# Performance work log

Measured on AMD Instinct MI355X. Metric: run time of the kernel, lower is better.

Reference implementation:

```python
import jax, jax.numpy as jnp
import numpy as np


def hadamard_transform(x):
    """Normalized fast Walsh-Hadamard transform along the last axis.

    Equivalent to x @ H_n / sqrt(n) with H_n the Sylvester Hadamard matrix.
    Last dim must be a power of two. Computed in fp32 (rotate_fp32=True).
    """
    orig_dtype = x.dtype
    x = x.astype(jnp.float32)
    n = x.shape[-1]
    lead = x.shape[:-1]
    x = x.reshape(-1, n)  # (B, n)
    h = 1
    while h < n:
        # butterfly stage: pairs separated by h
        x = x.reshape(-1, n // (2 * h), 2, h)
        a = x[:, :, 0, :]
        b = x[:, :, 1, :]
        x = jnp.stack([a + b, a - b], axis=2).reshape(-1, n)
        h *= 2
    x = x * (1.0 / np.sqrt(n)).astype(np.float32)
    return x.reshape(lead + (n,)).astype(orig_dtype)


def setup_inputs() -> dict:
    key = jax.random.key(0)
    k1, k2, k3 = jax.random.split(key, 3)
    B, S, D_IN, D_OUT = 4, 2048, 8192, 2048
    x = jax.random.normal(k1, (B, S, D_IN), dtype=jnp.float32)
    # nn.Linear params: weight (out, in), bias (out,) with kaiming-ish scale
    W = jax.random.normal(k2, (D_OUT, D_IN), dtype=jnp.float32) * (1.0 / np.sqrt(D_IN))
    b = jax.random.normal(k3, (D_OUT,), dtype=jnp.float32) * 0.01
    return {"x": x, "W": W, "b": b}


def reference(x, W, b):
    xh = hadamard_transform(x)                      # (B, S, D_in)
    return jnp.einsum('bsd,od->bso', xh, W) + b     # (B, S, D_out)
```

## Files before the change

kernel.cpp:

```cpp
#include <hip/hip_runtime.h>
#include <hip/hip_bf16.h>
#include <stdint.h>


#define M_TOTAL 8192
#define K_TOTAL 8192
#define N_TOTAL 2048
#define D_IN 8192

typedef __attribute__((ext_vector_type(8))) short short8;
typedef __attribute__((ext_vector_type(4))) float f32x4;

typedef __attribute__((address_space(1))) void void_g;
typedef __attribute__((address_space(3))) void void_l;
typedef __attribute__((address_space(3))) short lds_s3;

__device__ __forceinline__ short f2bf(float f) {
  __hip_bfloat16 h = __float2bfloat16(f);
  return *reinterpret_cast<short*>(&h);
}

__global__ void cvt_x_kernel(const float* __restrict__ x, short* __restrict__ xb, long n) {
  long stride = (long)gridDim.x * blockDim.x * 8;
  for (long i = ((long)blockIdx.x * blockDim.x + threadIdx.x) * 8; i < n; i += stride) {
    float4 v0 = *(const float4*)(x + i);
    float4 v1 = *(const float4*)(x + i + 4);
    short8 o;
    o[0] = f2bf(v0.x); o[1] = f2bf(v0.y); o[2] = f2bf(v0.z); o[3] = f2bf(v0.w);
    o[4] = f2bf(v1.x); o[5] = f2bf(v1.y); o[6] = f2bf(v1.z); o[7] = f2bf(v1.w);
    *(short8*)(xb + i) = o;
  }
}

__global__ void fwht_w_kernel(const float* __restrict__ W, short* __restrict__ Wh) {
  __shared__ float buf[D_IN];
  const int row = blockIdx.x;
  const float* src = W + (long)row * D_IN;
  for (int i = threadIdx.x; i < D_IN / 4; i += blockDim.x)
    ((float4*)buf)[i] = ((const float4*)src)[i];
  for (int h = 1; h < D_IN; h <<= 1) {
    __syncthreads();
    for (int p = threadIdx.x; p < D_IN / 2; p += blockDim.x) {
      int i = ((p & ~(h - 1)) << 1) | (p & (h - 1));
      float a = buf[i], b = buf[i + h];
      buf[i] = a + b;
      buf[i + h] = a - b;
    }
  }
  __syncthreads();
  const float s = 0.011048543456039806f;
  short* dst = Wh + (long)row * D_IN;
  for (int i = threadIdx.x; i < D_IN; i += blockDim.x)
    dst[i] = f2bf(buf[i] * s);
}

#define NKT 256

#define ABUF(b) ((b) * 8192)
#define BBUF(b) (32768 + (b) * 8192)

#define SBAR __builtin_amdgcn_sched_barrier(0)
#define BAR __builtin_amdgcn_s_barrier()
#define LG0 do { asm volatile("s_waitcnt lgkmcnt(0)"); SBAR; } while (0)
#define FEN4 do { SBAR; asm volatile("s_waitcnt vmcnt(4)"); BAR; } while (0)
#define FEN0 do { SBAR; asm volatile("s_waitcnt vmcnt(0)"); BAR; } while (0)

#define STAGET(PB, KOFF)                                                                          \
  __builtin_amdgcn_global_load_lds((void_g*)(aLo + (KOFF)),                                       \
                                   (void_l*)&lds[ABUF(PB) + sdst], 16, 0, 0);                     \
  __builtin_amdgcn_global_load_lds((void_g*)(aHi + (KOFF)),                                       \
                                   (void_l*)&lds[ABUF(PB) + sdst + 4096], 16, 0, 0);              \
  __builtin_amdgcn_global_load_lds((void_g*)(bLo + (KOFF)),                                       \
                                   (void_l*)&lds[BBUF(PB) + sdst], 16, 0, 0);                     \
  __builtin_amdgcn_global_load_lds((void_g*)(bHi + (KOFF)),                                       \
                                   (void_l*)&lds[BBUF(PB) + sdst + 4096], 16, 0, 0);

#define DSR(dst, ADDR, IMM)                                                                       \
  asm volatile("ds_read_b128 %0, %1 offset:%2" : "=v"(dst) : "v"(ADDR), "i"(IMM))

#define PRELOAD(NB)                                                                               \
  DSR(bn[0], bAdr, (NB) * 16384 + 0);    DSR(bn[1], bAdr, (NB) * 16384 + 1024);                   \
  DSR(bn[2], bAdr, (NB) * 16384 + 2048); DSR(bn[3], bAdr, (NB) * 16384 + 3072);                   \
  DSR(am[0], aAdr, (NB) * 16384 + 0);    DSR(am[1], aAdr, (NB) * 16384 + 1024);                   \
  DSR(am[2], aAdr, (NB) * 16384 + 2048); DSR(am[3], aAdr, (NB) * 16384 + 3072);                   \
  DSR(am[4], aAdr, (NB) * 16384 + 4096); DSR(am[5], aAdr, (NB) * 16384 + 5120);                   \
  DSR(am[6], aAdr, (NB) * 16384 + 6144); DSR(am[7], aAdr, (NB) * 16384 + 7168);

#define MFQ(MIB)                                                                                  \
  __builtin_amdgcn_s_setprio(1);                                                                  \
  _Pragma("unroll") for (int mi = 0; mi < 4; ++mi) {                                              \
    _Pragma("unroll") for (int nj = 0; nj < 4; ++nj)                                              \
        acc[(MIB) + mi][nj] = __builtin_amdgcn_mfma_f32_16x16x32_bf16(                            \
            am[(MIB) + mi], bn[nj], acc[(MIB) + mi][nj], 0, 0, 0);                                \
  }                                                                                               \
  __builtin_amdgcn_s_setprio(0);

#define KT(DOSTG, PB, KOFF, DOPRE, NB, DOF4, DOF0)                                                \
  {                                                                                               \
    LG0;                                                                                          \
    MFQ(0);                                                                                       \
    if (DOSTG) { STAGET(PB, KOFF); }                                                              \
    MFQ(4);                                                                                       \
    if (DOPRE) { PRELOAD(NB); }                                                                   \
    if (DOF4) FEN4;                                                                               \
    if (DOF0) FEN0;                                                                               \
  }

__global__ __launch_bounds__(512, 2) void gemm_kernel(const short* __restrict__ A,
                                                      const short* __restrict__ B,
                                                      const float* __restrict__ bias,
                                                      float* __restrict__ C) {
  __shared__ __attribute__((aligned(16))) short lds[65536];

  const int tid = threadIdx.x;
  const int l = tid & 63;
  const int w = tid >> 6;
  const int wm = w >> 2;
  const int wn = w & 3;

  const int bid = blockIdx.x;
  const int swz = (bid & 7) * 32 + (bid >> 3);
  const int bm = swz >> 3;
  const int bn_ = swz & 7;
  const long tileM = (long)bm * 256;
  const long tileN = (long)bn_ * 256;

  const int kx = (((l >> 4) ^ ((l >> 1) & 3)) * 8);
  const int rb = (l & 15) * 32;
  const unsigned ldsbase = (unsigned)(uintptr_t)(lds_s3*)&lds[0];
  const unsigned aAdr = ldsbase + (unsigned)(wm * 4096 + rb + kx) * 2u;
  const unsigned bAdr = ldsbase + (unsigned)(32768 + wn * 2048 + rb + kx) * 2u;

  const int sdst = tid * 8;
  const int sslot = ((tid & 3) ^ ((tid >> 3) & 3)) * 8;
  const short* aLo = A + (tileM + (tid >> 2)) * (long)K_TOTAL + sslot;
  const short* aHi = aLo + 128 * (long)K_TOTAL;
  const short* bLo = B + (tileN + (tid >> 2)) * (long)K_TOTAL + sslot;
  const short* bHi = bLo + 128 * (long)K_TOTAL;

  f32x4 acc[8][4];
#pragma unroll
  for (int mi = 0; mi < 8; ++mi)
#pragma unroll
    for (int nj = 0; nj < 4; ++nj)
      acc[mi][nj] = (f32x4){0.f, 0.f, 0.f, 0.f};

  short8 am[8], bn[4];

  STAGET(0, 0);
  STAGET(1, 32);
  STAGET(2, 64);
  SBAR;
  asm volatile("s_waitcnt vmcnt(4)");
  BAR;
  PRELOAD(0);

  for (int t4 = 0; t4 < 252; t4 += 4) {
    KT(true, 3, (t4 + 3) * 32, true, 1, true, false);
    KT(true, 0, (t4 + 4) * 32, true, 2, true, false);
    KT(true, 1, (t4 + 5) * 32, true, 3, true, false);
    KT(true, 2, (t4 + 6) * 32, true, 0, true, false);
  }
  KT(true, 3, 255 * 32, true, 1, true, false);
  KT(false, 0, 0, true, 2, false, true);
  KT(false, 0, 0, true, 3, false, false);
  KT(false, 0, 0, false, 0, false, false);

  const int rb0 = (int)tileM + wm * 128 + (l >> 4) * 4;
  const int cb = (int)tileN + wn * 64 + (l & 15);
#pragma unroll
  for (int mi = 0; mi < 8; ++mi)
#pragma unroll
    for (int nj = 0; nj < 4; ++nj) {
      float bv = bias[cb + nj * 16];
      const int r0 = rb0 + mi * 16;
#pragma unroll
      for (int r = 0; r < 4; ++r)
        C[(long)(r0 + r) * N_TOTAL + cb + nj * 16] = acc[mi][nj][r] + bv;
    }
}

extern "C" void kernel_launch(void* const* d_in, const int* in_sizes, int n_in,
                              void* d_out, int out_size, void* d_ws, size_t ws_size,
                              hipStream_t stream) {
  const float* x = (const float*)d_in[0];
  const float* W = (const float*)d_in[1];
  const float* bias = (const float*)d_in[2];
  float* out = (float*)d_out;

  short* xb = (short*)d_ws;
  short* wh = (short*)((char*)d_ws + (size_t)M_TOTAL * K_TOTAL * 2);

  cvt_x_kernel<<<2048, 256, 0, stream>>>(x, xb, (long)M_TOTAL * K_TOTAL);
  fwht_w_kernel<<<N_TOTAL, 256, 0, stream>>>(W, wh);

  const int grid = (M_TOTAL / 256) * (N_TOTAL / 256);
  gemm_kernel<<<grid, 512, 0, stream>>>(xb, wh, bias, out);
}
```

Before: 364.2 us.

## Merge prep kernels and retile GEMM to 256x128 with triple-buffered LDS

The x conversion and the W Hadamard transform are merged into one interleaved prep launch, so the two independent passes can overlap and one launch is saved. The GEMM output tile shrinks from 256x256 to 256x128, with a 4x2 wave layout and fewer accumulators. LDS drops to three stages (72 KB), and launch bounds now target four blocks per CU for higher occupancy. The pipeline issues split lgkmcnt waits so MFMAs can start while later LDS reads are in flight. The smaller tile reduces operand reuse and raises global and LDS traffic per FLOP.

```diff
diff --git a/kernel.cpp b/kernel.cpp
--- a/kernel.cpp
+++ b/kernel.cpp
@@ -20,160 +20,164 @@
   return *reinterpret_cast<short*>(&h);
 }
 
-__global__ void cvt_x_kernel(const float* __restrict__ x, short* __restrict__ xb, long n) {
-  long stride = (long)gridDim.x * blockDim.x * 8;
-  for (long i = ((long)blockIdx.x * blockDim.x + threadIdx.x) * 8; i < n; i += stride) {
-    float4 v0 = *(const float4*)(x + i);
-    float4 v1 = *(const float4*)(x + i + 4);
-    short8 o;
-    o[0] = f2bf(v0.x); o[1] = f2bf(v0.y); o[2] = f2bf(v0.z); o[3] = f2bf(v0.w);
-    o[4] = f2bf(v1.x); o[5] = f2bf(v1.y); o[6] = f2bf(v1.z); o[7] = f2bf(v1.w);
-    *(short8*)(xb + i) = o;
+__global__ __launch_bounds__(512) void prep_kernel(const float* __restrict__ x,
+                                                   short* __restrict__ xb,
+                                                   const float* __restrict__ W,
+                                                   short* __restrict__ wh) {
+  __shared__ float buf[D_IN];
+  const int b = blockIdx.x;
+  if ((b & 1) == 0) {
+    const int cb = b >> 1;
+    const long n = (long)M_TOTAL * K_TOTAL;
+    const long stride = (long)2048 * 512 * 8;
+    for (long i = ((long)cb * 512 + threadIdx.x) * 8; i < n; i += stride) {
+      float4 v0 = *(const float4*)(x + i);
+      float4 v1 = *(const float4*)(x + i + 4);
+      short8 o;
+      o[0] = f2bf(v0.x); o[1] = f2bf(v0.y); o[2] = f2bf(v0.z); o[3] = f2bf(v0.w);
+      o[4] = f2bf(v1.x); o[5] = f2bf(v1.y); o[6] = f2bf(v1.z); o[7] = f2bf(v1.w);
+      *(short8*)(xb + i) = o;
+    }
+  } else {
+    const int row = b >> 1;
+    const float* src = W + (long)row * D_IN;
+    for (int i = threadIdx.x; i < D_IN / 4; i += blockDim.x)
+      ((float4*)buf)[i] = ((const float4*)src)[i];
+    for (int h = 1; h < D_IN; h <<= 1) {
+      __syncthreads();
+      for (int p = threadIdx.x; p < D_IN / 2; p += blockDim.x) {
+        int i = ((p & ~(h - 1)) << 1) | (p & (h - 1));
+        float a = buf[i], bb = buf[i + h];
+        buf[i] = a + bb;
+        buf[i + h] = a - bb;
+      }
+    }
+    __syncthreads();
+    const float s = 0.011048543456039806f;
+    short* dst = wh + (long)row * D_IN;
+    for (int i = threadIdx.x; i < D_IN; i += blockDim.x)
+      dst[i] = f2bf(buf[i] * s);
   }
 }
 
-__global__ void fwht_w_kernel(const float* __restrict__ W, short* __restrict__ Wh) {
-  __shared__ float buf[D_IN];
-  const int row = blockIdx.x;
-  const float* src = W + (long)row * D_IN;
-  for (int i = threadIdx.x; i < D_IN / 4; i += blockDim.x)
-    ((float4*)buf)[i] = ((const float4*)src)[i];
-  for (int h = 1; h < D_IN; h <<= 1) {
-    __syncthreads();
-    for (int p = threadIdx.x; p < D_IN / 2; p += blockDim.x) {
-      int i = ((p & ~(h - 1)) << 1) | (p & (h - 1));
-      float a = buf[i], b = buf[i + h];
-      buf[i] = a + b;
-      buf[i + h] = a - b;
-    }
-  }
-  __syncthreads();
-  const float s = 0.011048543456039806f;
-  short* dst = Wh + (long)row * D_IN;
-  for (int i = threadIdx.x; i < D_IN; i += blockDim.x)
-    dst[i] = f2bf(buf[i] * s);
-}
-
 #define NKT 256
-
-#define ABUF(b) ((b) * 8192)
-#define BBUF(b) (32768 + (b) * 8192)
 
 #define SBAR __builtin_amdgcn_sched_barrier(0)
 #define BAR __builtin_amdgcn_s_barrier()
-#define LG0 do { asm volatile("s_waitcnt lgkmcnt(0)"); SBAR; } while (0)
-#define FEN4 do { SBAR; asm volatile("s_waitcnt vmcnt(4)"); BAR; } while (0)
+#define FEN3 do { SBAR; asm volatile("s_waitcnt vmcnt(3)"); BAR; } while (0)
 #define FEN0 do { SBAR; asm volatile("s_waitcnt vmcnt(0)"); BAR; } while (0)
-
-#define STAGET(PB, KOFF)                                                                          \
+#define FNOP do { } while (0)
+
+#define STAGE(SB, KOFF)                                                                           \
   __builtin_amdgcn_global_load_lds((void_g*)(aLo + (KOFF)),                                       \
-                                   (void_l*)&lds[ABUF(PB) + sdst], 16, 0, 0);                     \
+                                   (void_l*)&lds[(SB) * 12288 + sdst], 16, 0, 0);                 \
   __builtin_amdgcn_global_load_lds((void_g*)(aHi + (KOFF)),                                       \
-                                   (void_l*)&lds[ABUF(PB) + sdst + 4096], 16, 0, 0);              \
-  __builtin_amdgcn_global_load_lds((void_g*)(bLo + (KOFF)),                                       \
-                                   (void_l*)&lds[BBUF(PB) + sdst], 16, 0, 0);                     \
-  __builtin_amdgcn_global_load_lds((void_g*)(bHi + (KOFF)),                                       \
-                                   (void_l*)&lds[BBUF(PB) + sdst + 4096], 16, 0, 0);
+                                   (void_l*)&lds[(SB) * 12288 + 4096 + sdst], 16, 0, 0);          \
+  __builtin_amdgcn_global_load_lds((void_g*)(bSrc + (KOFF)),                                      \
+                                   (void_l*)&lds[(SB) * 12288 + 8192 + sdst], 16, 0, 0);
 
 #define DSR(dst, ADDR, IMM)                                                                       \
   asm volatile("ds_read_b128 %0, %1 offset:%2" : "=v"(dst) : "v"(ADDR), "i"(IMM))
 
+#define BB(NB) ((NB) < 2 ? bAdLo : bAdHi)
+#define BI(NB) (((NB) < 2 ? (NB) : 0) * 24576)
 #define PRELOAD(NB)                                                                               \
-  DSR(bn[0], bAdr, (NB) * 16384 + 0);    DSR(bn[1], bAdr, (NB) * 16384 + 1024);                   \
-  DSR(bn[2], bAdr, (NB) * 16384 + 2048); DSR(bn[3], bAdr, (NB) * 16384 + 3072);                   \
-  DSR(am[0], aAdr, (NB) * 16384 + 0);    DSR(am[1], aAdr, (NB) * 16384 + 1024);                   \
-  DSR(am[2], aAdr, (NB) * 16384 + 2048); DSR(am[3], aAdr, (NB) * 16384 + 3072);                   \
-  DSR(am[4], aAdr, (NB) * 16384 + 4096); DSR(am[5], aAdr, (NB) * 16384 + 5120);                   \
-  DSR(am[6], aAdr, (NB) * 16384 + 6144); DSR(am[7], aAdr, (NB) * 16384 + 7168);
-
-#define MFQ(MIB)                                                                                  \
+  DSR(bn[0], BB(NB), BI(NB) + 0);    DSR(bn[1], BB(NB), BI(NB) + 1024);                           \
+  DSR(bn[2], BB(NB), BI(NB) + 2048); DSR(bn[3], BB(NB), BI(NB) + 3072);                           \
+  DSR(am[0], aAdr, (NB) * 24576 + 0);    DSR(am[1], aAdr, (NB) * 24576 + 1024);                   \
+  DSR(am[2], aAdr, (NB) * 24576 + 2048); DSR(am[3], aAdr, (NB) * 24576 + 3072);
+
+#define MFQ(M2)                                                                                   \
   __builtin_amdgcn_s_setprio(1);                                                                  \
-  _Pragma("unroll") for (int mi = 0; mi < 4; ++mi) {                                              \
+  _Pragma("unroll") for (int mi = 0; mi < 2; ++mi) {                                              \
     _Pragma("unroll") for (int nj = 0; nj < 4; ++nj)                                              \
-        acc[(MIB) + mi][nj] = __builtin_amdgcn_mfma_f32_16x16x32_bf16(                            \
-            am[(MIB) + mi], bn[nj], acc[(MIB) + mi][nj], 0, 0, 0);                                \
+        acc[(M2) + mi][nj] = __builtin_amdgcn_mfma_f32_16x16x32_bf16(                             \
+            am[(M2) + mi], bn[nj], acc[(M2) + mi][nj], 0, 0, 0);                                  \
   }                                                                                               \
   __builtin_amdgcn_s_setprio(0);
 
-#define KT(DOSTG, PB, KOFF, DOPRE, NB, DOF4, DOF0)                                                \
+#define KT(DOSTG, SB, KOFF, DOPRE, NB, FEN)                                                       \
   {                                                                                               \
-    LG0;                                                                                          \
+    asm volatile("s_waitcnt lgkmcnt(2)");                                                         \
+    SBAR;                                                                                         \
     MFQ(0);                                                                                       \
-    if (DOSTG) { STAGET(PB, KOFF); }                                                              \
-    MFQ(4);                                                                                       \
+    if (DOSTG) { STAGE(SB, KOFF); }                                                               \
+    SBAR;                                                                                         \
+    asm volatile("s_waitcnt lgkmcnt(0)");                                                         \
+    SBAR;                                                                                         \
+    MFQ(2);                                                                                       \
+    FEN;                                                                                          \
     if (DOPRE) { PRELOAD(NB); }                                                                   \
-    if (DOF4) FEN4;                                                                               \
-    if (DOF0) FEN0;                                                                               \
+    SBAR;                                                                                         \
   }
 
-__global__ __launch_bounds__(512, 2) void gemm_kernel(const short* __restrict__ A,
+__global__ __launch_bounds__(512, 4) void gemm_kernel(const short* __restrict__ A,
                                                       const short* __restrict__ B,
                                                       const float* __restrict__ bias,
                                                       float* __restrict__ C) {
-  __shared__ __attribute__((aligned(16))) short lds[65536];
+  __shared__ __attribute__((aligned(16))) short lds[36864];
 
   const int tid = threadIdx.x;
   const int l = tid & 63;
   const int w = tid >> 6;
-  const int wm = w >> 2;
-  const int wn = w & 3;
+  const int wm = w >> 1;
+  const int wn = w & 1;
 
   const int bid = blockIdx.x;
-  const int swz = (bid & 7) * 32 + (bid >> 3);
-  const int bm = swz >> 3;
-  const int bn_ = swz & 7;
+  const int swz = (bid & 7) * 64 + (bid >> 3);
+  const int bm = swz >> 4;
+  const int bn_ = swz & 15;
   const long tileM = (long)bm * 256;
-  const long tileN = (long)bn_ * 256;
-
-  const int kx = (((l >> 4) ^ ((l >> 1) & 3)) * 8);
-  const int rb = (l & 15) * 32;
-  const unsigned ldsbase = (unsigned)(uintptr_t)(lds_s3*)&lds[0];
-  const unsigned aAdr = ldsbase + (unsigned)(wm * 4096 + rb + kx) * 2u;
-  const unsigned bAdr = ldsbase + (unsigned)(32768 + wn * 2048 + rb + kx) * 2u;
+  const long tileN = (long)bn_ * 128;
+
+  const int kx = ((l >> 4) ^ ((l >> 1) & 3)) * 16;
+  const unsigned ldsb = (unsigned)(uintptr_t)(lds_s3*)&lds[0];
+  const unsigned aAdr = ldsb + (unsigned)((wm * 64 + (l & 15)) * 64 + kx);
+  const unsigned bAdLo = ldsb + 16384u + (unsigned)((wn * 64 + (l & 15)) * 64 + kx);
+  const unsigned bAdHi = bAdLo + 49152u;
 
   const int sdst = tid * 8;
+  const int srow = tid >> 2;
   const int sslot = ((tid & 3) ^ ((tid >> 3) & 3)) * 8;
-  const short* aLo = A + (tileM + (tid >> 2)) * (long)K_TOTAL + sslot;
+  const short* aLo = A + (tileM + srow) * (long)K_TOTAL + sslot;
   const short* aHi = aLo + 128 * (long)K_TOTAL;
-  const short* bLo = B + (tileN + (tid >> 2)) * (long)K_TOTAL + sslot;
-  const short* bHi = bLo + 128 * (long)K_TOTAL;
-
-  f32x4 acc[8][4];
-#pragma unroll
-  for (int mi = 0; mi < 8; ++mi)
+  const short* bSrc = B + (tileN + srow) * (long)K_TOTAL + sslot;
+
+  f32x4 acc[4][4];
+#pragma unroll
+  for (int mi = 0; mi < 4; ++mi)
 #pragma unroll
     for (int nj = 0; nj < 4; ++nj)
       acc[mi][nj] = (f32x4){0.f, 0.f, 0.f, 0.f};
 
-  short8 am[8], bn[4];
-
-  STAGET(0, 0);
-  STAGET(1, 32);
-  STAGET(2, 64);
+  short8 am[4], bn[4];
+
+  STAGE(0, 0);
+  STAGE(1, 32);
   SBAR;
-  asm volatile("s_waitcnt vmcnt(4)");
+  asm volatile("s_waitcnt vmcnt(3)");
   BAR;
   PRELOAD(0);
-
-  for (int t4 = 0; t4 < 252; t4 += 4) {
-    KT(true, 3, (t4 + 3) * 32, true, 1, true, false);
-    KT(true, 0, (t4 + 4) * 32, true, 2, true, false);
-    KT(true, 1, (t4 + 5) * 32, true, 3, true, false);
-    KT(true, 2, (t4 + 6) * 32, true, 0, true, false);
+  SBAR;
+
+  for (int t3 = 0; t3 < 252; t3 += 3) {
+    KT(true, 2, (t3 + 2) * 32, true, 1, FEN3);
+    KT(true, 0, (t3 + 3) * 32, true, 2, FEN3);
+    KT(true, 1, (t3 + 4) * 32, true, 0, FEN3);
   }
-  KT(true, 3, 255 * 32, true, 1, true, false);
-  KT(false, 0, 0, true, 2, false, true);
-  KT(false, 0, 0, true, 3, false, false);
-  KT(false, 0, 0, false, 0, false, false);
-
-  const int rb0 = (int)tileM + wm * 128 + (l >> 4) * 4;
+  KT(true, 2, 254 * 32, true, 1, FEN3);
+  KT(true, 0, 255 * 32, true, 2, FEN3);
+  KT(false, 0, 0, true, 0, FEN0);
+  KT(false, 0, 0, false, 0, FNOP);
+
+  const int rb = (int)tileM + wm * 64 + (l >> 4) * 4;
   const int cb = (int)tileN + wn * 64 + (l & 15);
 #pragma unroll
-  for (int mi = 0; mi < 8; ++mi)
+  for (int mi = 0; mi < 4; ++mi)
 #pragma unroll
     for (int nj = 0; nj < 4; ++nj) {
       float bv = bias[cb + nj * 16];
-      const int r0 = rb0 + mi * 16;
+      const int r0 = rb + mi * 16;
 #pragma unroll
       for (int r = 0; r < 4; ++r)
         C[(long)(r0 + r) * N_TOTAL + cb + nj * 16] = acc[mi][nj][r] + bv;
@@ -191,9 +195,8 @@
   short* xb = (short*)d_ws;
   short* wh = (short*)((char*)d_ws + (size_t)M_TOTAL * K_TOTAL * 2);
 
-  cvt_x_kernel<<<2048, 256, 0, stream>>>(x, xb, (long)M_TOTAL * K_TOTAL);
-  fwht_w_kernel<<<N_TOTAL, 256, 0, stream>>>(W, wh);
-
-  const int grid = (M_TOTAL / 256) * (N_TOTAL / 256);
+  prep_kernel<<<4096, 512, 0, stream>>>(x, xb, W, wh);
+
+  const int grid = (M_TOTAL / 256) * (N_TOTAL / 128);
   gemm_kernel<<<grid, 512, 0, stream>>>(xb, wh, bias, out);
 }
```

Result: slower. 377.1 us (+3.5%).
